# Performance work log

Measured on AMD Instinct MI355X. Metric: run time of the kernel, lower is better.

## Reference

```python
import jax, jax.numpy as jnp
import numpy as np

EMBED_DIM = 1024
NUM_HEADS = 16
HEAD_DIM = EMBED_DIM // NUM_HEADS
SEQ_LEN = 2048
BATCH = 2


def setup_inputs() -> dict:
    key = jax.random.key(0)
    ks = jax.random.split(key, 9)
    s = 1.0 / np.sqrt(EMBED_DIM)
    inputs = jax.random.normal(ks[0], (BATCH, SEQ_LEN, EMBED_DIM), dtype=jnp.float32)
    Wq = jax.random.uniform(ks[1], (EMBED_DIM, EMBED_DIM), jnp.float32, -s, s)
    bq = jax.random.uniform(ks[2], (EMBED_DIM,), jnp.float32, -s, s)
    Wk = jax.random.uniform(ks[3], (EMBED_DIM, EMBED_DIM), jnp.float32, -s, s)
    bk = jax.random.uniform(ks[4], (EMBED_DIM,), jnp.float32, -s, s)
    Wv = jax.random.uniform(ks[5], (EMBED_DIM, EMBED_DIM), jnp.float32, -s, s)
    bv = jax.random.uniform(ks[6], (EMBED_DIM,), jnp.float32, -s, s)
    Wo = jax.random.uniform(ks[7], (EMBED_DIM, EMBED_DIM), jnp.float32, -s, s)
    bo = jax.random.uniform(ks[8], (EMBED_DIM,), jnp.float32, -s, s)
    return {"inputs": inputs, "Wq": Wq, "bq": bq, "Wk": Wk, "bk": bk,
            "Wv": Wv, "bv": bv, "Wo": Wo, "bo": bo}


def reference(inputs, Wq, bq, Wk, bk, Wv, bv, Wo, bo):
    B, S, D = inputs.shape
    H, Hd = NUM_HEADS, HEAD_DIM

    def heads(x):  # [B,S,D] -> [B,H,S,Hd]
        return x.reshape(B, S, H, Hd).transpose(0, 2, 1, 3)

    q = heads(inputs @ Wq + bq)
    k = heads(inputs @ Wk + bk)
    v = heads(inputs @ Wv + bv)

    # [B,H,S,S] causal scores (naive, matching original module)
    scores = jnp.einsum('bhqd,bhkd->bhqk', q, k) * (Hd ** -0.5)
    causal = jnp.tril(jnp.ones((S, S), dtype=bool))
    scores = jnp.where(causal, scores, jnp.float32(-jnp.inf))
    attn = jax.nn.softmax(scores, axis=-1)

    out = jnp.einsum('bhqk,bhkd->bhqd', attn, v)
    out = out.transpose(0, 2, 1, 3).reshape(B, S, D)
    return out @ Wo + bo
```

## Files before the change

### kernel.cpp

```cpp
#include <hip/hip_runtime.h>
#include <stdint.h>
#include <stddef.h>

#define SEQ   2048
#define DIM   1024
#define NH    16
#define HD    64
#define MTOT  4096
#define LPAD  72
#define EPAD  136
#define FPAD  132

typedef __attribute__((ext_vector_type(8))) short short8;
typedef __attribute__((ext_vector_type(4))) float floatx4;
typedef __attribute__((ext_vector_type(4))) float float4v;
typedef __attribute__((ext_vector_type(4))) unsigned short ushort4v;

__device__ __forceinline__ floatx4 mfma_bf16(short8 a, short8 b, floatx4 c) {
    return __builtin_amdgcn_mfma_f32_16x16x32_bf16(a, b, c, 0, 0, 0);
}

__device__ __forceinline__ float b2f(unsigned short s) {
    unsigned int u = ((unsigned int)s) << 16;
    return __builtin_bit_cast(float, u);
}
__device__ __forceinline__ unsigned short f2b(float f) {
    unsigned int u = __builtin_bit_cast(unsigned int, f);
    u += 0x7fffu + ((u >> 16) & 1u);
    return (unsigned short)(u >> 16);
}

__global__ __launch_bounds__(256) void cvt_f32_bf16(const float* __restrict__ in,
                                                    unsigned short* __restrict__ out) {
    const int i = (blockIdx.x * 256 + threadIdx.x) * 4;
    const float4v v = *(const float4v*)&in[i];
    ushort4v o;
    o.x = f2b(v.x); o.y = f2b(v.y); o.z = f2b(v.z); o.w = f2b(v.w);
    *(ushort4v*)&out[i] = o;
}

__global__ __launch_bounds__(256) void transpose_all(const float* __restrict__ w0,
                                                     const float* __restrict__ w1,
                                                     const float* __restrict__ w2,
                                                     const float* __restrict__ w3,
                                                     unsigned short* __restrict__ outbase) {
    __shared__ float t[64][65];
    const int z = blockIdx.z;
    const float* in = (z == 0) ? w0 : (z == 1) ? w1 : (z == 2) ? w2 : w3;
    unsigned short* out = outbase + (size_t)z * DIM * DIM;
    const int c0 = blockIdx.x * 64, r0 = blockIdx.y * 64;
    const int x = threadIdx.x, y = threadIdx.y;
#pragma unroll
    for (int i = 0; i < 64; i += 4)
        t[y + i][x] = in[(size_t)(r0 + y + i) * DIM + c0 + x];
    __syncthreads();
#pragma unroll
    for (int i = 0; i < 64; i += 4)
        out[(size_t)(c0 + y + i) * DIM + r0 + x] = f2b(t[x][y + i]);
}

__global__ __launch_bounds__(256) void gemm_fused(const unsigned short* __restrict__ A,
                                                  const unsigned short* __restrict__ WTbase,
                                                  const float* __restrict__ b0,
                                                  const float* __restrict__ b1,
                                                  const float* __restrict__ b2,
                                                  void* __restrict__ outbase,
                                                  int qkv) {
    __shared__ __attribute__((aligned(16))) unsigned short smem[2 * 128 * LPAD];
    unsigned short* As = smem;
    unsigned short* Bs = smem + 128 * LPAD;

    const int z = blockIdx.z;
    const unsigned short* BT = WTbase + (size_t)z * (DIM * DIM);
    const float* bias        = (z == 0) ? b0 : (z == 1) ? b1 : b2;
    const int mode = qkv ? ((z == 0) ? 1 : (z == 1) ? 3 : 4) : 0;
    float* Cf          = (float*)outbase;
    unsigned short* Cb = (unsigned short*)outbase + (size_t)z * ((size_t)MTOT * DIM);

    const int tid = threadIdx.x;
    const int w = tid >> 6, lane = tid & 63;
    const int quad = lane >> 4, l16 = lane & 15;
    const int wm = w >> 1, wn = w & 1;
    const int m0 = blockIdx.x * 128, n0 = blockIdx.y * 128;
    const int bb = m0 >> 11;

    floatx4 acc[4][4];
#pragma unroll
    for (int mi = 0; mi < 4; ++mi)
#pragma unroll
        for (int ni = 0; ni < 4; ++ni) acc[mi][ni] = (floatx4)0.0f;

    const int srow = tid >> 3, scol = (tid & 7) * 8;

    short8 pa[4], pb[4];
#pragma unroll
    for (int ch = 0; ch < 4; ++ch) {
        pa[ch] = *(const short8*)&A[(size_t)(m0 + ch * 32 + srow) * DIM + scol];
        pb[ch] = *(const short8*)&BT[(size_t)(n0 + ch * 32 + srow) * DIM + scol];
    }

    for (int k0 = 0;; k0 += 64) {
#pragma unroll
        for (int ch = 0; ch < 4; ++ch) {
            *(short8*)&As[(ch * 32 + srow) * LPAD + scol] = pa[ch];
            *(short8*)&Bs[(ch * 32 + srow) * LPAD + scol] = pb[ch];
        }
        __syncthreads();
        const bool more = (k0 + 64 < DIM);
        if (more) {
#pragma unroll
            for (int ch = 0; ch < 4; ++ch) {
                pa[ch] = *(const short8*)&A[(size_t)(m0 + ch * 32 + srow) * DIM + k0 + 64 + scol];
                pb[ch] = *(const short8*)&BT[(size_t)(n0 + ch * 32 + srow) * DIM + k0 + 64 + scol];
            }
        }
#pragma unroll
        for (int kk = 0; kk < 2; ++kk) {
            short8 a[4], b[4];
#pragma unroll
            for (int mi = 0; mi < 4; ++mi)
                a[mi] = *(const short8*)&As[(wm * 64 + mi * 16 + l16) * LPAD + kk * 32 + quad * 8];
#pragma unroll
            for (int ni = 0; ni < 4; ++ni)
                b[ni] = *(const short8*)&Bs[(wn * 64 + ni * 16 + l16) * LPAD + kk * 32 + quad * 8];
#pragma unroll
            for (int mi = 0; mi < 4; ++mi)
#pragma unroll
                for (int ni = 0; ni < 4; ++ni)
                    acc[mi][ni] = mfma_bf16(a[mi], b[ni], acc[mi][ni]);
        }
        if (!more) break;
        __syncthreads();
    }

    float bvv[4];
#pragma unroll
    for (int ni = 0; ni < 4; ++ni) bvv[ni] = bias[n0 + wn * 64 + ni * 16 + l16];

    if (mode == 0) {
        float* T = (float*)smem;
        for (int p = 0; p < 4; ++p) {
            __syncthreads();
            if (wm == (p >> 1)) {
                const int mib = (p & 1) * 2;
#pragma unroll
                for (int mm = 0; mm < 2; ++mm)
#pragma unroll
                    for (int ni = 0; ni < 4; ++ni)
#pragma unroll
                        for (int r = 0; r < 4; ++r)
                            T[(mm * 16 + quad * 4 + r) * FPAD + wn * 64 + ni * 16 + l16] =
                                acc[mib + mm][ni][r] + bvv[ni];
            }
            __syncthreads();
#pragma unroll
            for (int it = 0; it < 4; ++it) {
                const int c = it * 256 + tid;
                const int row = c >> 5, nof = (c & 31) * 4;
                *(float4v*)&Cf[(size_t)(m0 + p * 32 + row) * DIM + n0 + nof] =
                    *(const float4v*)&T[row * FPAD + nof];
            }
        }
    } else if (mode == 1) {
        unsigned short* T = smem;
        __syncthreads();
#pragma unroll
        for (int mi = 0; mi < 4; ++mi)
#pragma unroll
            for (int ni = 0; ni < 4; ++ni)
#pragma unroll
                for (int r = 0; r < 4; ++r)
                    T[(wm * 64 + mi * 16 + quad * 4 + r) * EPAD + wn * 64 + ni * 16 + l16] =
                        f2b(acc[mi][ni][r] + bvv[ni]);
        __syncthreads();
#pragma unroll
        for (int it = 0; it < 8; ++it) {
            const int c = it * 256 + tid;
            const int seg = c >> 3, d8 = (c & 7) * 8;
            const int mm = seg >> 1, hseg = seg & 1;
            const int h = (n0 >> 6) + hseg;
            const int s = (m0 & (SEQ - 1)) + mm;
            *(short8*)&Cb[((size_t)(bb * NH + h) * SEQ + s) * HD + d8] =
                *(const short8*)&T[mm * EPAD + hseg * 64 + d8];
        }
    } else if (mode == 3) {
        unsigned short* T = smem;
        __syncthreads();
#pragma unroll
        for (int mi = 0; mi < 4; ++mi)
#pragma unroll
            for (int ni = 0; ni < 4; ++ni)
#pragma unroll
                for (int r = 0; r < 4; ++r)
                    T[(wm * 64 + mi * 16 + quad * 4 + r) * EPAD + wn * 64 + ni * 16 + l16] =
                        f2b(acc[mi][ni][r] + bvv[ni]);
        __syncthreads();
#pragma unroll
        for (int it = 0; it < 8; ++it) {
            const int f = it * 256 + tid;
            const int ln = f & 63, fragid = f >> 6;
            const int h2 = fragid >> 4, j2 = (fragid >> 3) & 1;
            const int ni = (fragid >> 1) & 3, kk = fragid & 1;
            const int l16f = ln & 15, quadf = ln >> 4;
            const short8 v = *(const short8*)&T[(j2 * 64 + ni * 16 + l16f) * EPAD +
                                               h2 * 64 + kk * 32 + quadf * 8];
            const int bh = bb * NH + (n0 >> 6) + h2;
            const int jg = ((m0 & (SEQ - 1)) >> 6) + j2;
            *(short8*)&Cb[(((size_t)bh * 32 + jg) * 8 + ni * 2 + kk) * 512 + ln * 8] = v;
        }
    } else {
        unsigned short* T = smem;
        __syncthreads();
#pragma unroll
        for (int mi = 0; mi < 4; ++mi)
#pragma unroll
            for (int ni = 0; ni < 4; ++ni) {
                ushort4v pk;
#pragma unroll
                for (int r = 0; r < 4; ++r) pk[r] = f2b(acc[mi][ni][r] + bvv[ni]);
                *(ushort4v*)&T[(wn * 64 + ni * 16 + l16) * EPAD + wm * 64 + mi * 16 + quad * 4] = pk;
            }
        __syncthreads();
#pragma unroll
        for (int it = 0; it < 8; ++it) {
            const int f = it * 256 + tid;
            const int ln = f & 63, fragid = f >> 6;
            const int h2 = fragid >> 4, j2 = (fragid >> 3) & 1;
            const int ni = (fragid >> 1) & 3, kk = fragid & 1;
            const int l16f = ln & 15, quadf = ln >> 4;
            const short8 v = *(const short8*)&T[(h2 * 64 + ni * 16 + l16f) * EPAD +
                                               j2 * 64 + kk * 32 + quadf * 8];
            const int bh = bb * NH + (n0 >> 6) + h2;
            const int jg = ((m0 & (SEQ - 1)) >> 6) + j2;
            *(short8*)&Cb[(((size_t)bh * 32 + jg) * 8 + ni * 2 + kk) * 512 + ln * 8] = v;
        }
    }
}

__global__ __launch_bounds__(64) void attn_fwd(const unsigned short* __restrict__ Q,
                                               const unsigned short* __restrict__ KP,
                                               const unsigned short* __restrict__ VP,
                                               unsigned short* __restrict__ O) {
    __shared__ __attribute__((aligned(16))) unsigned short Os[32 * LPAD];

    const int bh = blockIdx.x;
    const int qc = (gridDim.y - 1) - blockIdx.y;
    const int lane = threadIdx.x;
    const int quad = lane >> 4, l16 = lane & 15;

    const unsigned short* Qh  = Q  + (size_t)bh * SEQ * HD;
    const unsigned short* KPh = KP + (size_t)bh * 32 * 4096;
    const unsigned short* VPh = VP + (size_t)bh * 32 * 4096;
    const int q0 = qc * 32;
    const int jend = qc >> 1;

    short8 qf[2][2];
#pragma unroll
    for (int mi = 0; mi < 2; ++mi)
#pragma unroll
        for (int kk = 0; kk < 2; ++kk) {
            short8 t = *(const short8*)(Qh + (size_t)(q0 + mi * 16 + l16) * HD + kk * 32 + quad * 8);
            short8 o;
#pragma unroll
            for (int e = 0; e < 8; ++e)
                o[e] = (short)f2b(b2f((unsigned short)t[e]) * 0.125f);
            qf[mi][kk] = o;
        }

    short8 ones;
#pragma unroll
    for (int e = 0; e < 8; ++e) ones[e] = (short)0x3F80;

    floatx4 o_acc[2][4], l_acc[2];
#pragma unroll
    for (int mi = 0; mi < 2; ++mi) {
#pragma unroll
        for (int ni = 0; ni < 4; ++ni) o_acc[mi][ni] = (floatx4)0.0f;
        l_acc[mi] = (floatx4)0.0f;
    }

    for (int j = 0; j <= jend; ++j) {
        const unsigned short* kb = KPh + (size_t)j * 4096 + lane * 8;
        const unsigned short* vb = VPh + (size_t)j * 4096 + lane * 8;
        short8 kf[4][2], vf[4][2];
#pragma unroll
        for (int ni = 0; ni < 4; ++ni)
#pragma unroll
            for (int kk = 0; kk < 2; ++kk) {
                kf[ni][kk] = *(const short8*)(kb + (ni * 2 + kk) * 512);
                vf[ni][kk] = *(const short8*)(vb + (ni * 2 + kk) * 512);
            }

        floatx4 s_acc[2][4];
#pragma unroll
        for (int mi = 0; mi < 2; ++mi)
#pragma unroll
            for (int ni = 0; ni < 4; ++ni) s_acc[mi][ni] = (floatx4)0.0f;
#pragma unroll
        for (int kk = 0; kk < 2; ++kk)
#pragma unroll
            for (int ni = 0; ni < 4; ++ni)
#pragma unroll
                for (int mi = 0; mi < 2; ++mi)
                    s_acc[mi][ni] = mfma_bf16(qf[mi][kk], kf[ni][kk], s_acc[mi][ni]);

#pragma unroll
        for (int mi = 0; mi < 2; ++mi) {
            float p[4][4];
#pragma unroll
            for (int r = 0; r < 4; ++r) {
                const int q = q0 + mi * 16 + quad * 4 + r;
#pragma unroll
                for (int ni = 0; ni < 4; ++ni) {
                    const int key = j * 64 + ni * 16 + l16;
                    p[ni][r] = (key > q) ? 0.0f : __expf(s_acc[mi][ni][r]);
                }
            }
#pragma unroll
            for (int ni = 0; ni < 4; ++ni)
#pragma unroll
                for (int r = 0; r < 4; ++r)
                    Os[(quad * 4 + r) * LPAD + ni * 16 + l16] = f2b(p[ni][r]);

#pragma unroll
            for (int kk = 0; kk < 2; ++kk) {
                const short8 pfrag = *(const short8*)&Os[l16 * LPAD + kk * 32 + quad * 8];
#pragma unroll
                for (int ni = 0; ni < 4; ++ni)
                    o_acc[mi][ni] = mfma_bf16(pfrag, vf[ni][kk], o_acc[mi][ni]);
                l_acc[mi] = mfma_bf16(pfrag, ones, l_acc[mi]);
            }
        }
    }

    float inv[2][4];
#pragma unroll
    for (int mi = 0; mi < 2; ++mi)
#pragma unroll
        for (int r = 0; r < 4; ++r) inv[mi][r] = 1.0f / l_acc[mi][r];
#pragma unroll
    for (int mi = 0; mi < 2; ++mi)
#pragma unroll
        for (int ni = 0; ni < 4; ++ni)
#pragma unroll
            for (int r = 0; r < 4; ++r)
                Os[(mi * 16 + quad * 4 + r) * LPAD + ni * 16 + l16] =
                    f2b(o_acc[mi][ni][r] * inv[mi][r]);
    const int bb = bh >> 4, h = bh & 15;
#pragma unroll
    for (int it = 0; it < 4; ++it) {
        const int row = it * 8 + (lane >> 3), d8 = (lane & 7) * 8;
        *(short8*)&O[(size_t)(bb * SEQ + q0 + row) * DIM + h * HD + d8] =
            *(const short8*)&Os[row * LPAD + d8];
    }
}

extern "C" void kernel_launch(void* const* d_in, const int* in_sizes, int n_in,
                              void* d_out, int out_size, void* d_ws, size_t ws_size,
                              hipStream_t stream) {
    const float* X  = (const float*)d_in[0];
    const float* Wq = (const float*)d_in[1];
    const float* bq = (const float*)d_in[2];
    const float* Wk = (const float*)d_in[3];
    const float* bk = (const float*)d_in[4];
    const float* Wv = (const float*)d_in[5];
    const float* bv = (const float*)d_in[6];
    const float* Wo = (const float*)d_in[7];
    const float* bo = (const float*)d_in[8];

    unsigned short* ws = (unsigned short*)d_ws;
    const size_t WSZ = (size_t)DIM * DIM;
    const size_t TSZ = (size_t)MTOT * DIM;
    unsigned short* WqT = ws;
    unsigned short* WoT = ws + 3 * WSZ;
    unsigned short* Qb  = ws + 4 * WSZ;
    unsigned short* Kp  = Qb + TSZ;
    unsigned short* Vp  = Kp + TSZ;
    unsigned short* Ob  = Vp + TSZ;

    unsigned short* Xb = (unsigned short*)d_out;

    cvt_f32_bf16<<<dim3(TSZ / 1024), 256, 0, stream>>>(X, Xb);

    transpose_all<<<dim3(16, 16, 4), dim3(64, 4), 0, stream>>>(Wq, Wk, Wv, Wo, WqT);

    gemm_fused<<<dim3(MTOT / 128, DIM / 128, 3), 256, 0, stream>>>(
        Xb, WqT, bq, bk, bv, (void*)Qb, 1);

    attn_fwd<<<dim3(2 * NH, SEQ / 32), 64, 0, stream>>>(Qb, Kp, Vp, Ob);

    gemm_fused<<<dim3(MTOT / 128, DIM / 128, 1), 256, 0, stream>>>(
        Ob, WoT, bo, bo, bo, d_out, 0);
}
```

Measured before the change: 200.5 us.

## Rewrite attention kernel with 32x32 MFMA, transposed scores and register-resident P

The attention kernel moves from 16x16x32 to 32x32x16 bf16 MFMA and computes S^T = K·Q so each lane holds one query's scores. P is packed with v_cvt_pk_bf16_f32 and rearranged with v_permlane32_swap, which removes the LDS round-trip for P and the ones-MFMA used for row sums. K/V blocks shrink to 32 keys, are double-buffered in registers, and only the diagonal block is masked. The projection epilogue writes K/V in the new 32-row fragment layout, adding coupling between the kernels.

Measured after the change: 186.3 us. -7.1%, faster.

```diff
diff --git a/kernel.cpp b/kernel.cpp
--- a/kernel.cpp
+++ b/kernel.cpp
@@ -13,11 +13,16 @@
 
 typedef __attribute__((ext_vector_type(8))) short short8;
 typedef __attribute__((ext_vector_type(4))) float floatx4;
+typedef __attribute__((ext_vector_type(16))) float floatx16;
 typedef __attribute__((ext_vector_type(4))) float float4v;
 typedef __attribute__((ext_vector_type(4))) unsigned short ushort4v;
+typedef __attribute__((ext_vector_type(4))) unsigned int uint4v;
 
 __device__ __forceinline__ floatx4 mfma_bf16(short8 a, short8 b, floatx4 c) {
     return __builtin_amdgcn_mfma_f32_16x16x32_bf16(a, b, c, 0, 0, 0);
+}
+__device__ __forceinline__ floatx16 mfma32(short8 a, short8 b, floatx16 c) {
+    return __builtin_amdgcn_mfma_f32_32x32x16_bf16(a, b, c, 0, 0, 0);
 }
 
 __device__ __forceinline__ float b2f(unsigned short s) {
@@ -28,6 +33,19 @@
     unsigned int u = __builtin_bit_cast(unsigned int, f);
     u += 0x7fffu + ((u >> 16) & 1u);
     return (unsigned short)(u >> 16);
+}
+__device__ __forceinline__ unsigned int cvtpk(float lo, float hi) {
+    unsigned int w;
+    asm("v_cvt_pk_bf16_f32 %0, %1, %2" : "=v"(w) : "v"(lo), "v"(hi));
+    return w;
+}
+__device__ __forceinline__ void swap32(unsigned int& a, unsigned int& b) {
+    asm("v_permlane32_swap_b32 %0, %1" : "+v"(a), "+v"(b));
+}
+__device__ __forceinline__ short8 mk8(unsigned int a, unsigned int b,
+                                      unsigned int c, unsigned int d) {
+    uint4v u; u.x = a; u.y = b; u.z = c; u.w = d;
+    return __builtin_bit_cast(short8, u);
 }
 
 __global__ __launch_bounds__(256) void cvt_f32_bf16(const float* __restrict__ in,
@@ -199,14 +217,14 @@
         for (int it = 0; it < 8; ++it) {
             const int f = it * 256 + tid;
             const int ln = f & 63, fragid = f >> 6;
-            const int h2 = fragid >> 4, j2 = (fragid >> 3) & 1;
-            const int ni = (fragid >> 1) & 3, kk = fragid & 1;
-            const int l16f = ln & 15, quadf = ln >> 4;
-            const short8 v = *(const short8*)&T[(j2 * 64 + ni * 16 + l16f) * EPAD +
-                                               h2 * 64 + kk * 32 + quadf * 8];
+            const int h2 = fragid >> 4;
+            const int jb = (fragid >> 2) & 3;
+            const int c  = fragid & 3;
+            const short8 v = *(const short8*)&T[(jb * 32 + (ln & 31)) * EPAD +
+                                                h2 * 64 + c * 16 + (ln >> 5) * 8];
             const int bh = bb * NH + (n0 >> 6) + h2;
-            const int jg = ((m0 & (SEQ - 1)) >> 6) + j2;
-            *(short8*)&Cb[(((size_t)bh * 32 + jg) * 8 + ni * 2 + kk) * 512 + ln * 8] = v;
+            const int jg = ((m0 & (SEQ - 1)) >> 5) + jb;
+            *(short8*)&Cb[(((size_t)bh * 64 + jg) * 4 + c) * 512 + ln * 8] = v;
         }
     } else {
         unsigned short* T = smem;
@@ -225,14 +243,15 @@
         for (int it = 0; it < 8; ++it) {
             const int f = it * 256 + tid;
             const int ln = f & 63, fragid = f >> 6;
-            const int h2 = fragid >> 4, j2 = (fragid >> 3) & 1;
-            const int ni = (fragid >> 1) & 3, kk = fragid & 1;
-            const int l16f = ln & 15, quadf = ln >> 4;
-            const short8 v = *(const short8*)&T[(h2 * 64 + ni * 16 + l16f) * EPAD +
-                                               j2 * 64 + kk * 32 + quadf * 8];
+            const int h2 = fragid >> 4;
+            const int jb = (fragid >> 2) & 3;
+            const int dk = fragid & 3;
+            const int d0 = dk >> 1, kk = dk & 1;
+            const short8 v = *(const short8*)&T[(h2 * 64 + d0 * 32 + (ln & 31)) * EPAD +
+                                                jb * 32 + kk * 16 + (ln >> 5) * 8];
             const int bh = bb * NH + (n0 >> 6) + h2;
-            const int jg = ((m0 & (SEQ - 1)) >> 6) + j2;
-            *(short8*)&Cb[(((size_t)bh * 32 + jg) * 8 + ni * 2 + kk) * 512 + ln * 8] = v;
+            const int jg = ((m0 & (SEQ - 1)) >> 5) + jb;
+            *(short8*)&Cb[(((size_t)bh * 64 + jg) * 4 + dk) * 512 + ln * 8] = v;
         }
     }
 }
@@ -242,110 +261,106 @@
                                                const unsigned short* __restrict__ VP,
                                                unsigned short* __restrict__ O) {
     __shared__ __attribute__((aligned(16))) unsigned short Os[32 * LPAD];
+    __shared__ float Linv[32];
 
     const int bh = blockIdx.x;
     const int qc = (gridDim.y - 1) - blockIdx.y;
     const int lane = threadIdx.x;
-    const int quad = lane >> 4, l16 = lane & 15;
+    const int ql  = lane & 31;
+    const int hi  = lane >> 5;
+    const int hi4 = hi * 4;
+    const int hi8 = hi * 8;
 
     const unsigned short* Qh  = Q  + (size_t)bh * SEQ * HD;
-    const unsigned short* KPh = KP + (size_t)bh * 32 * 4096;
-    const unsigned short* VPh = VP + (size_t)bh * 32 * 4096;
+    const unsigned short* KPh = KP + (size_t)bh * (64 * 2048);
+    const unsigned short* VPh = VP + (size_t)bh * (64 * 2048);
     const int q0 = qc * 32;
-    const int jend = qc >> 1;
-
-    short8 qf[2][2];
-#pragma unroll
-    for (int mi = 0; mi < 2; ++mi)
-#pragma unroll
-        for (int kk = 0; kk < 2; ++kk) {
-            short8 t = *(const short8*)(Qh + (size_t)(q0 + mi * 16 + l16) * HD + kk * 32 + quad * 8);
-            short8 o;
-#pragma unroll
-            for (int e = 0; e < 8; ++e)
-                o[e] = (short)f2b(b2f((unsigned short)t[e]) * 0.125f);
-            qf[mi][kk] = o;
-        }
-
-    short8 ones;
-#pragma unroll
-    for (int e = 0; e < 8; ++e) ones[e] = (short)0x3F80;
-
-    floatx4 o_acc[2][4], l_acc[2];
-#pragma unroll
-    for (int mi = 0; mi < 2; ++mi) {
-#pragma unroll
-        for (int ni = 0; ni < 4; ++ni) o_acc[mi][ni] = (floatx4)0.0f;
-        l_acc[mi] = (floatx4)0.0f;
-    }
-
-    for (int j = 0; j <= jend; ++j) {
-        const unsigned short* kb = KPh + (size_t)j * 4096 + lane * 8;
-        const unsigned short* vb = VPh + (size_t)j * 4096 + lane * 8;
-        short8 kf[4][2], vf[4][2];
-#pragma unroll
-        for (int ni = 0; ni < 4; ++ni)
-#pragma unroll
-            for (int kk = 0; kk < 2; ++kk) {
-                kf[ni][kk] = *(const short8*)(kb + (ni * 2 + kk) * 512);
-                vf[ni][kk] = *(const short8*)(vb + (ni * 2 + kk) * 512);
-            }
-
-        floatx4 s_acc[2][4];
-#pragma unroll
-        for (int mi = 0; mi < 2; ++mi)
-#pragma unroll
-            for (int ni = 0; ni < 4; ++ni) s_acc[mi][ni] = (floatx4)0.0f;
-#pragma unroll
-        for (int kk = 0; kk < 2; ++kk)
-#pragma unroll
-            for (int ni = 0; ni < 4; ++ni)
-#pragma unroll
-                for (int mi = 0; mi < 2; ++mi)
-                    s_acc[mi][ni] = mfma_bf16(qf[mi][kk], kf[ni][kk], s_acc[mi][ni]);
-
-#pragma unroll
-        for (int mi = 0; mi < 2; ++mi) {
-            float p[4][4];
-#pragma unroll
-            for (int r = 0; r < 4; ++r) {
-                const int q = q0 + mi * 16 + quad * 4 + r;
-#pragma unroll
-                for (int ni = 0; ni < 4; ++ni) {
-                    const int key = j * 64 + ni * 16 + l16;
-                    p[ni][r] = (key > q) ? 0.0f : __expf(s_acc[mi][ni][r]);
-                }
-            }
-#pragma unroll
-            for (int ni = 0; ni < 4; ++ni)
-#pragma unroll
-                for (int r = 0; r < 4; ++r)
-                    Os[(quad * 4 + r) * LPAD + ni * 16 + l16] = f2b(p[ni][r]);
-
-#pragma unroll
-            for (int kk = 0; kk < 2; ++kk) {
-                const short8 pfrag = *(const short8*)&Os[l16 * LPAD + kk * 32 + quad * 8];
-#pragma unroll
-                for (int ni = 0; ni < 4; ++ni)
-                    o_acc[mi][ni] = mfma_bf16(pfrag, vf[ni][kk], o_acc[mi][ni]);
-                l_acc[mi] = mfma_bf16(pfrag, ones, l_acc[mi]);
-            }
-        }
-    }
-
-    float inv[2][4];
-#pragma unroll
-    for (int mi = 0; mi < 2; ++mi)
-#pragma unroll
-        for (int r = 0; r < 4; ++r) inv[mi][r] = 1.0f / l_acc[mi][r];
-#pragma unroll
-    for (int mi = 0; mi < 2; ++mi)
-#pragma unroll
-        for (int ni = 0; ni < 4; ++ni)
-#pragma unroll
-            for (int r = 0; r < 4; ++r)
-                Os[(mi * 16 + quad * 4 + r) * LPAD + ni * 16 + l16] =
-                    f2b(o_acc[mi][ni][r] * inv[mi][r]);
+
+    short8 qf[4];
+#pragma unroll
+    for (int c = 0; c < 4; ++c) {
+        short8 t = *(const short8*)(Qh + (size_t)(q0 + ql) * HD + c * 16 + hi8);
+        short8 o;
+#pragma unroll
+        for (int e = 0; e < 8; ++e)
+            o[e] = (short)f2b(b2f((unsigned short)t[e]) * 0.125f);
+        qf[c] = o;
+    }
+
+    floatx16 o_acc0 = (floatx16)0.0f, o_acc1 = (floatx16)0.0f;
+    float l0 = 0.0f, l1 = 0.0f;
+
+#define LOADKV(KF, VF, JJ) do {                                              \
+        const unsigned short* kb_ = KPh + (size_t)(JJ) * 2048 + lane * 8;    \
+        const unsigned short* vb_ = VPh + (size_t)(JJ) * 2048 + lane * 8;    \
+        _Pragma("unroll")                                                    \
+        for (int c_ = 0; c_ < 4; ++c_) {                                     \
+            KF[c_] = *(const short8*)(kb_ + c_ * 512);                       \
+            VF[c_] = *(const short8*)(vb_ + c_ * 512);                       \
+        }                                                                    \
+    } while (0)
+
+#define ATT_BLOCK(KF, VF, MASKED) do {                                       \
+        floatx16 st_ = (floatx16)0.0f;                                       \
+        _Pragma("unroll")                                                    \
+        for (int c_ = 0; c_ < 4; ++c_) st_ = mfma32(KF[c_], qf[c_], st_);    \
+        float p_[16];                                                        \
+        _Pragma("unroll")                                                    \
+        for (int r_ = 0; r_ < 16; ++r_) {                                    \
+            float e_ = __expf(st_[r_]);                                      \
+            if (MASKED)                                                      \
+                e_ = (((r_ & 3) + 8 * (r_ >> 2) + hi4) > ql) ? 0.0f : e_;    \
+            p_[r_] = e_;                                                     \
+        }                                                                    \
+        l0 += (p_[0] + p_[1]) + (p_[2] + p_[3]);                             \
+        l1 += (p_[4] + p_[5]) + (p_[6] + p_[7]);                             \
+        l0 += (p_[8] + p_[9]) + (p_[10] + p_[11]);                           \
+        l1 += (p_[12] + p_[13]) + (p_[14] + p_[15]);                         \
+        unsigned int w0_ = cvtpk(p_[0], p_[1]),   w2_ = cvtpk(p_[4], p_[5]); \
+        unsigned int w1_ = cvtpk(p_[2], p_[3]),   w3_ = cvtpk(p_[6], p_[7]); \
+        unsigned int w4_ = cvtpk(p_[8], p_[9]),   w6_ = cvtpk(p_[12], p_[13]); \
+        unsigned int w5_ = cvtpk(p_[10], p_[11]), w7_ = cvtpk(p_[14], p_[15]); \
+        swap32(w0_, w2_); swap32(w1_, w3_);                                  \
+        swap32(w4_, w6_); swap32(w5_, w7_);                                  \
+        const short8 pa0_ = mk8(w0_, w1_, w2_, w3_);                         \
+        const short8 pa1_ = mk8(w4_, w5_, w6_, w7_);                         \
+        o_acc0 = mfma32(pa0_, VF[0], o_acc0);                                \
+        o_acc0 = mfma32(pa1_, VF[1], o_acc0);                                \
+        o_acc1 = mfma32(pa0_, VF[2], o_acc1);                                \
+        o_acc1 = mfma32(pa1_, VF[3], o_acc1);                                \
+    } while (0)
+
+    short8 kfA[4], vfA[4], kfB[4], vfB[4];
+    LOADKV(kfA, vfA, 0);
+    int j = 0;
+    while (j + 2 <= qc) {
+        LOADKV(kfB, vfB, j + 1);
+        ATT_BLOCK(kfA, vfA, 0);
+        LOADKV(kfA, vfA, j + 2);
+        ATT_BLOCK(kfB, vfB, 0);
+        j += 2;
+    }
+    if (j < qc) {
+        LOADKV(kfB, vfB, qc);
+        ATT_BLOCK(kfA, vfA, 0);
+        ATT_BLOCK(kfB, vfB, 1);
+    } else {
+        ATT_BLOCK(kfA, vfA, 1);
+    }
+
+    float l = l0 + l1;
+    l += __shfl_xor(l, 32, 64);
+    const float inv = 1.0f / l;
+    if (lane < 32) Linv[lane] = inv;
+    __syncthreads();
+#pragma unroll
+    for (int r = 0; r < 16; ++r) {
+        const int row = (r & 3) + 8 * (r >> 2) + hi4;
+        const float iv = Linv[row];
+        Os[row * LPAD + ql]      = f2b(o_acc0[r] * iv);
+        Os[row * LPAD + 32 + ql] = f2b(o_acc1[r] * iv);
+    }
+    __syncthreads();
     const int bb = bh >> 4, h = bh & 15;
 #pragma unroll
     for (int it = 0; it < 4; ++it) {
@@ -353,6 +368,8 @@
         *(short8*)&O[(size_t)(bb * SEQ + q0 + row) * DIM + h * HD + d8] =
             *(const short8*)&Os[row * LPAD + d8];
     }
+#undef LOADKV
+#undef ATT_BLOCK
 }
 
 extern "C" void kernel_launch(void* const* d_in, const int* in_sizes, int n_in,
```
